# Kernel tuning notes

Measured on AMD Instinct MI355X. Metric: run time of the kernel, lower is better.

The kernel has to match this reference:

```python
import jax, jax.numpy as jnp
import numpy as np

B, N, C, H = 2, 2048, 1024, 16
D = C // H  # head_dim = 64
EPS = 1e-6


def rmsnorm(x, w, eps=EPS):
    # RMSNorm over last dim (head_dim), matching torch RMSNorm (computed in fp32)
    x32 = x.astype(jnp.float32)
    y = x32 * jax.lax.rsqrt(jnp.mean(x32 * x32, axis=-1, keepdims=True) + eps)
    return y.astype(x.dtype) * w


def setup_inputs() -> dict:
    key = jax.random.key(0)
    ks = jax.random.split(key, 4)
    return {
        "x": jax.random.normal(ks[0], (B, N, C), dtype=jnp.float32),
        "w_qkv": jax.random.normal(ks[1], (C, 3 * C), dtype=jnp.float32) * 0.02,
        "b_qkv": jnp.zeros((3 * C,), dtype=jnp.float32),
        "q_w": jnp.ones((D,), dtype=jnp.float32),
        "k_w": jnp.ones((D,), dtype=jnp.float32),
        "w_proj": jax.random.normal(ks[2], (C, C), dtype=jnp.float32) * 0.02,
        "b_proj": jnp.zeros((C,), dtype=jnp.float32),
    }


def reference(x, w_qkv, b_qkv, q_w, k_w, w_proj, b_proj):
    b, n, c = x.shape
    h, d = H, c // H
    # QKV projection -> [3, B, H, N, D]
    qkv = (x @ w_qkv + b_qkv).reshape(b, n, 3, h, d).transpose(2, 0, 3, 1, 4)
    q, k, v = qkv[0], qkv[1], qkv[2]
    # per-head RMSNorm on q/k (qk_norm=True, use_rmsnorm=True)
    q = rmsnorm(q, q_w)
    k = rmsnorm(k, k_w)
    # scaled dot-product attention (scale = head_dim**-0.5, no dropout at eval)
    scale = d ** -0.5
    attn = jax.nn.softmax(jnp.einsum('bhqd,bhkd->bhqk', q, k) * scale, axis=-1)
    out = jnp.einsum('bhqk,bhkd->bhqd', attn, v)  # [B,H,N,D]
    out = out.transpose(0, 2, 1, 3).reshape(b, n, c)
    return out @ w_proj + b_proj
```

## Files before the change

kernel.cpp:

```cpp
#include <hip/hip_runtime.h>

typedef unsigned short u16;
typedef unsigned int u32;
typedef float f4 __attribute__((ext_vector_type(4)));
typedef __bf16 b8 __attribute__((ext_vector_type(8)));
typedef _Float16 h4 __attribute__((ext_vector_type(4)));
typedef __fp16 hp2 __attribute__((ext_vector_type(2)));

#if __has_builtin(__builtin_amdgcn_exp2f)
#define EXP2(x) __builtin_amdgcn_exp2f(x)
#else
#define EXP2(x) exp2f(x)
#endif

__device__ __forceinline__ u16 f2bf(float f) {
  unsigned u = __float_as_uint(f);
  u += 0x7fffu + ((u >> 16) & 1u);
  return (u16)(u >> 16);
}
__device__ __forceinline__ float bf2f(u16 h) {
  return __uint_as_float(((unsigned)h) << 16);
}

__global__ void k_convert_all(const float* __restrict__ x,
                              const float* __restrict__ w_qkv,
                              const float* __restrict__ w_proj,
                              u16* __restrict__ xb, u16* __restrict__ wqkT,
                              u16* __restrict__ wpjT) {
  __shared__ u16 t[64][65];
  int bid = blockIdx.x;
  if (bid < 2048) {
    int i = (bid * 256 + threadIdx.x) * 8;
    float4 a = *(const float4*)(x + i);
    float4 b = *(const float4*)(x + i + 4);
    union { u16 h[8]; uint4 v; } r;
    r.h[0] = f2bf(a.x); r.h[1] = f2bf(a.y); r.h[2] = f2bf(a.z); r.h[3] = f2bf(a.w);
    r.h[4] = f2bf(b.x); r.h[5] = f2bf(b.y); r.h[6] = f2bf(b.z); r.h[7] = f2bf(b.w);
    *(uint4*)(xb + i) = r.v;
    return;
  }
  const float* w; u16* wT; int Ncols, Krows, bx, by;
  if (bid < 2816) { int l = bid - 2048; w = w_qkv; wT = wqkT; Ncols = 3072; Krows = 1024; bx = l % 48; by = l / 48; }
  else            { int l = bid - 2816; w = w_proj; wT = wpjT; Ncols = 1024; Krows = 1024; bx = l & 15; by = l >> 4; }
  int n0 = bx * 64, k0 = by * 64;
#pragma unroll
  for (int it = 0; it < 16; ++it) {
    int e = it * 256 + threadIdx.x;
    int r = e >> 6, c = e & 63;
    t[r][c] = f2bf(w[(size_t)(k0 + r) * Ncols + n0 + c]);
  }
  __syncthreads();
#pragma unroll
  for (int it = 0; it < 16; ++it) {
    int e = it * 256 + threadIdx.x;
    int r = e >> 6, c = e & 63;
    wT[(size_t)(n0 + r) * Krows + k0 + c] = t[c][r];
  }
}

__global__ __launch_bounds__(256, 3) void k_gemm_qkv(
    const u16* __restrict__ A, const u16* __restrict__ Bt,
    const float* __restrict__ bias,
    u16* __restrict__ oq, u16* __restrict__ ok, u16* __restrict__ ov,
    const float* __restrict__ qw, const float* __restrict__ kw,
    int K) {
  __shared__ u16 lA[128 * 32];
  __shared__ u16 lB[128 * 32];
  const int tid = threadIdx.x;
  const int lane = tid & 63, lrow = lane & 15, lq = lane >> 4;
  const int wave = tid >> 6;
  const int bm = blockIdx.y * 128, bn = blockIdx.x * 128;
  const int wm = (wave >> 1) * 64, wn = (wave & 1) * 64;

  const int ch0 = tid, ch1 = 256 + tid;
  const u16* ap0 = A + (size_t)(bm + (ch0 >> 2)) * K + (ch0 & 3) * 8;
  const u16* ap1 = A + (size_t)(bm + (ch1 >> 2)) * K + (ch1 & 3) * 8;
  const u16* bp0 = Bt + (size_t)(bn + (ch0 >> 2)) * K + (ch0 & 3) * 8;
  const u16* bp1 = Bt + (size_t)(bn + (ch1 >> 2)) * K + (ch1 & 3) * 8;
  u16* lAw0 = lA + ch0 * 8; u16* lAw1 = lA + ch1 * 8;
  u16* lBw0 = lB + ch0 * 8; u16* lBw1 = lB + ch1 * 8;

  uint4 pA0 = *(const uint4*)ap0, pA1 = *(const uint4*)ap1;
  uint4 pB0 = *(const uint4*)bp0, pB1 = *(const uint4*)bp1;

  f4 acc[4][4] = {};
  const int iters = K >> 5;
  for (int it = 0; it < iters; ++it) {
    *(uint4*)lAw0 = pA0; *(uint4*)lAw1 = pA1;
    *(uint4*)lBw0 = pB0; *(uint4*)lBw1 = pB1;
    __syncthreads();
    if (it + 1 < iters) {
      ap0 += 32; ap1 += 32; bp0 += 32; bp1 += 32;
      pA0 = *(const uint4*)ap0; pA1 = *(const uint4*)ap1;
      pB0 = *(const uint4*)bp0; pB1 = *(const uint4*)bp1;
    }
    b8 af[4], bf[4];
#pragma unroll
    for (int i = 0; i < 4; ++i)
      af[i] = *(const b8*)(lA + (wm + i * 16 + lrow) * 32 + lq * 8);
#pragma unroll
    for (int j = 0; j < 4; ++j)
      bf[j] = *(const b8*)(lB + (wn + j * 16 + lrow) * 32 + lq * 8);
#pragma unroll
    for (int i = 0; i < 4; ++i)
#pragma unroll
      for (int j = 0; j < 4; ++j)
        acc[i][j] = __builtin_amdgcn_mfma_f32_16x16x32_bf16(af[i], bf[j], acc[i][j], 0, 0, 0);
    __syncthreads();
  }

  float bv[4];
#pragma unroll
  for (int j = 0; j < 4; ++j) bv[j] = bias[bn + wn + j * 16 + lrow];

  const float CS = 0.125f * 1.44269504088896340736f;
  const int n0w = bn + wn;
  const int sec = n0w >> 10;
  const int h = (n0w >> 6) & 15;
#pragma unroll
  for (int i = 0; i < 4; ++i) {
    float v[4][4];
#pragma unroll
    for (int j = 0; j < 4; ++j)
#pragma unroll
      for (int r = 0; r < 4; ++r) v[j][r] = acc[i][j][r] + bv[j];
    if (sec < 2) {
      u16* dst = sec == 0 ? oq : ok;
      const float* w = sec == 0 ? qw : kw;
      float ex = sec == 0 ? CS : 1.0f;
#pragma unroll
      for (int r = 0; r < 4; ++r) {
        float ss = v[0][r] * v[0][r] + v[1][r] * v[1][r] +
                   v[2][r] * v[2][r] + v[3][r] * v[3][r];
        ss += __shfl_xor(ss, 1, 64); ss += __shfl_xor(ss, 2, 64);
        ss += __shfl_xor(ss, 4, 64); ss += __shfl_xor(ss, 8, 64);
        float sc = rsqrtf(ss * (1.0f / 64.0f) + 1e-6f) * ex;
        int m = bm + wm + i * 16 + lq * 4 + r;
        int bb = m >> 11, ns = m & 2047;
        u16* rowp = dst + ((size_t)(bb * 16 + h) * 2048 + ns) * 64;
#pragma unroll
        for (int j = 0; j < 4; ++j) {
          int d = j * 16 + lrow;
          rowp[d] = f2bf(v[j][r] * sc * w[d]);
        }
      }
    } else {
      int m0 = bm + wm + i * 16 + lq * 4;
      int bb = m0 >> 11, ns = m0 & 2047;
#pragma unroll
      for (int j = 0; j < 4; ++j) {
        int d = j * 16 + lrow;
        union { _Float16 hh[4]; uint2 u; } pk;
#pragma unroll
        for (int r = 0; r < 4; ++r) pk.hh[r] = (_Float16)v[j][r];
        *(uint2*)(ov + ((size_t)(bb * 16 + h) * 64 + d) * 2048 + ns) = pk.u;
      }
    }
  }
}

__global__ __launch_bounds__(256, 4) void k_gemm2(
    const u16* __restrict__ A, const u16* __restrict__ Bt,
    const float* __restrict__ bias, float* __restrict__ outF,
    int K, int Ncols) {
  __shared__ u16 lA[64 * 32];
  __shared__ u16 lB[128 * 32];
  const int tid = threadIdx.x;
  const int lane = tid & 63, lrow = lane & 15, lq = lane >> 4;
  const int wave = tid >> 6;
  const int bm = blockIdx.y * 64, bn = blockIdx.x * 128;
  const int wm = (wave >> 1) * 32, wn = (wave & 1) * 64;

  const int cha = tid;
  const int ch0 = tid, ch1 = 256 + tid;
  const u16* ap = A + (size_t)(bm + (cha >> 2)) * K + (cha & 3) * 8;
  const u16* bp0 = Bt + (size_t)(bn + (ch0 >> 2)) * K + (ch0 & 3) * 8;
  const u16* bp1 = Bt + (size_t)(bn + (ch1 >> 2)) * K + (ch1 & 3) * 8;
  u16* lAw = lA + cha * 8;
  u16* lBw0 = lB + ch0 * 8; u16* lBw1 = lB + ch1 * 8;

  uint4 pA = *(const uint4*)ap;
  uint4 pB0 = *(const uint4*)bp0, pB1 = *(const uint4*)bp1;

  f4 acc[2][4] = {};
  const int iters = K >> 5;
  for (int it = 0; it < iters; ++it) {
    *(uint4*)lAw = pA;
    *(uint4*)lBw0 = pB0; *(uint4*)lBw1 = pB1;
    __syncthreads();
    if (it + 1 < iters) {
      ap += 32; bp0 += 32; bp1 += 32;
      pA = *(const uint4*)ap;
      pB0 = *(const uint4*)bp0; pB1 = *(const uint4*)bp1;
    }
    b8 af[2], bf[4];
#pragma unroll
    for (int i = 0; i < 2; ++i)
      af[i] = *(const b8*)(lA + (wm + i * 16 + lrow) * 32 + lq * 8);
#pragma unroll
    for (int j = 0; j < 4; ++j)
      bf[j] = *(const b8*)(lB + (wn + j * 16 + lrow) * 32 + lq * 8);
#pragma unroll
    for (int i = 0; i < 2; ++i)
#pragma unroll
      for (int j = 0; j < 4; ++j)
        acc[i][j] = __builtin_amdgcn_mfma_f32_16x16x32_bf16(af[i], bf[j], acc[i][j], 0, 0, 0);
    __syncthreads();
  }
#pragma unroll
  for (int i = 0; i < 2; ++i)
#pragma unroll
    for (int j = 0; j < 4; ++j) {
      int n = bn + wn + j * 16 + lrow;
      float bv = bias[n];
#pragma unroll
      for (int r = 0; r < 4; ++r) {
        int m = bm + wm + i * 16 + lq * 4 + r;
        outF[(size_t)m * Ncols + n] = acc[i][j][r] + bv;
      }
    }
}

__global__ __launch_bounds__(512, 4) void k_attn(
    const u16* __restrict__ qb, const u16* __restrict__ kb,
    const u16* __restrict__ vt, u16* __restrict__ ao) {
  __shared__ u16 lK[128 * 72];
  __shared__ u16 lV[64 * 140];
  const int bh = blockIdx.y;
  const int q0 = blockIdx.x * 128;
  const int tid = threadIdx.x, wave = tid >> 6, lane = tid & 63;
  const int lrow = lane & 15, lq = lane >> 4;
  const int wq = wave * 16;

  b8 qf[2];
#pragma unroll
  for (int ks = 0; ks < 2; ++ks)
    qf[ks] = *(const b8*)(qb + ((size_t)bh * 2048 + q0 + wq + lrow) * 64 + ks * 32 + lq * 8);

  f4 o[4] = {};
  f4 lacc = {};
  h4 ones;
  ones[0] = (_Float16)1.0f; ones[1] = (_Float16)1.0f;
  ones[2] = (_Float16)1.0f; ones[3] = (_Float16)1.0f;

  const int ch0 = tid, ch1 = 512 + tid;
  const u16* kp0 = kb + (size_t)bh * 2048 * 64 + (size_t)(ch0 >> 3) * 64 + (ch0 & 7) * 8;
  const u16* kp1 = kb + (size_t)bh * 2048 * 64 + (size_t)(ch1 >> 3) * 64 + (ch1 & 7) * 8;
  const u16* vp0 = vt + (size_t)bh * 64 * 2048 + (size_t)(ch0 >> 4) * 2048 + (ch0 & 15) * 8;
  const u16* vp1 = vt + (size_t)bh * 64 * 2048 + (size_t)(ch1 >> 4) * 2048 + (ch1 & 15) * 8;
  u16* lKw0 = lK + (ch0 >> 3) * 72 + (ch0 & 7) * 8;
  u16* lKw1 = lK + (ch1 >> 3) * 72 + (ch1 & 7) * 8;
  u16* lVw0 = lV + (ch0 >> 4) * 140 + (ch0 & 15) * 8;
  u16* lVw1 = lV + (ch1 >> 4) * 140 + (ch1 & 15) * 8;

  uint4 pK0, pK1, pV0, pV1;
  pK0 = *(const uint4*)kp0; pK1 = *(const uint4*)kp1;
  pV0 = *(const uint4*)vp0; pV1 = *(const uint4*)vp1;

  for (int it = 0; it < 16; ++it) {
    *(uint4*)lKw0 = pK0;
    *(uint4*)lKw1 = pK1;
    *(uint2*)lVw0 = make_uint2(pV0.x, pV0.y);
    *(uint2*)(lVw0 + 4) = make_uint2(pV0.z, pV0.w);
    *(uint2*)lVw1 = make_uint2(pV1.x, pV1.y);
    *(uint2*)(lVw1 + 4) = make_uint2(pV1.z, pV1.w);
    __syncthreads();

    if (it < 15) {
      kp0 += 128 * 64; kp1 += 128 * 64; vp0 += 128; vp1 += 128;
      pK0 = *(const uint4*)kp0; pK1 = *(const uint4*)kp1;
      pV0 = *(const uint4*)vp0; pV1 = *(const uint4*)vp1;
    }

    f4 st[8] = {};
#pragma unroll
    for (int ks = 0; ks < 2; ++ks)
#pragma unroll
      for (int kt = 0; kt < 8; ++kt) {
        b8 kf = *(const b8*)(lK + (kt * 16 + lrow) * 72 + ks * 32 + lq * 8);
        st[kt] = __builtin_amdgcn_mfma_f32_16x16x32_bf16(kf, qf[ks], st[kt], 0, 0, 0);
      }

    h4 pf[8];
#pragma unroll
    for (int kt = 0; kt < 8; ++kt) {
      union { hp2 p2[2]; h4 v; } cv;
      cv.p2[0] = __builtin_amdgcn_cvt_pkrtz(EXP2(st[kt][0]), EXP2(st[kt][1]));
      cv.p2[1] = __builtin_amdgcn_cvt_pkrtz(EXP2(st[kt][2]), EXP2(st[kt][3]));
      pf[kt] = cv.v;
    }

#pragma unroll
    for (int kt = 0; kt < 8; ++kt) {
      lacc = __builtin_amdgcn_mfma_f32_16x16x16f16(ones, pf[kt], lacc, 0, 0, 0);
#pragma unroll
      for (int dt = 0; dt < 4; ++dt) {
        h4 va = *(const h4*)(lV + (dt * 16 + lrow) * 140 + kt * 16 + lq * 4);
        o[dt] = __builtin_amdgcn_mfma_f32_16x16x16f16(va, pf[kt], o[dt], 0, 0, 0);
      }
    }
    __syncthreads();
  }

  float inv = 1.0f / lacc[0];

  const int bb = bh >> 4, h = bh & 15;
  int q = q0 + wq + lrow;
#pragma unroll
  for (int dt = 0; dt < 4; ++dt) {
    union { u16 h2[4]; uint2 v; } r;
#pragma unroll
    for (int rr = 0; rr < 4; ++rr) r.h2[rr] = f2bf(o[dt][rr] * inv);
    *(uint2*)(ao + ((size_t)bb * 2048 + q) * 1024 + h * 64 + dt * 16 + lq * 4) = r.v;
  }
}

extern "C" void kernel_launch(void* const* d_in, const int* in_sizes, int n_in,
                              void* d_out, int out_size, void* d_ws, size_t ws_size,
                              hipStream_t stream) {
  const float* x      = (const float*)d_in[0];
  const float* w_qkv  = (const float*)d_in[1];
  const float* b_qkv  = (const float*)d_in[2];
  const float* q_w    = (const float*)d_in[3];
  const float* k_w    = (const float*)d_in[4];
  const float* w_proj = (const float*)d_in[5];
  const float* b_proj = (const float*)d_in[6];
  float* out = (float*)d_out;

  u16* xb   = (u16*)d_ws;
  u16* wqkT = xb + 4194304;
  u16* wpjT = wqkT + 3145728;
  u16* qb   = wpjT + 1048576;
  u16* kb   = qb + 4194304;
  u16* vtb  = kb + 4194304;
  u16* ao   = xb;

  k_convert_all<<<3072, 256, 0, stream>>>(x, w_qkv, w_proj, xb, wqkT, wpjT);
  k_gemm_qkv<<<dim3(24, 32), 256, 0, stream>>>(xb, wqkT, b_qkv, qb, kb, vtb, q_w, k_w, 1024);
  k_attn<<<dim3(16, 32), 512, 0, stream>>>(qb, kb, vtb, ao);
  k_gemm2<<<dim3(8, 64), 256, 0, stream>>>(ao, wpjT, b_proj, out, 1024, 1024);
}
```

Baseline: 193.3 us.

## Double attention KV tile to 256 keys and vectorize weight transpose stores

The attention kernel now stages 256 keys of K and V per iteration instead of 128 and processes them in two halves. This halves the number of barrier pairs and loop iterations, and lengthens each register-prefetch batch. In exchange it uses more LDS per block, about 70KB, which can cut how many blocks fit on a CU, and it needs more prefetch registers. The weight-transpose kernel also packs four bf16 values into 8-byte stores instead of writing scalar 2-byte ones.

```diff
diff --git a/kernel.cpp b/kernel.cpp
--- a/kernel.cpp
+++ b/kernel.cpp
@@ -51,10 +51,13 @@
   }
   __syncthreads();
 #pragma unroll
-  for (int it = 0; it < 16; ++it) {
+  for (int it = 0; it < 4; ++it) {
     int e = it * 256 + threadIdx.x;
-    int r = e >> 6, c = e & 63;
-    wT[(size_t)(n0 + r) * Krows + k0 + c] = t[c][r];
+    int r = e >> 4, c0 = (e & 15) * 4;
+    union { u16 h[4]; uint2 v; } pk;
+    pk.h[0] = t[c0][r]; pk.h[1] = t[c0 + 1][r];
+    pk.h[2] = t[c0 + 2][r]; pk.h[3] = t[c0 + 3][r];
+    *(uint2*)(wT + (size_t)(n0 + r) * Krows + k0 + c0) = pk.v;
   }
 }
 
@@ -224,8 +227,8 @@
 __global__ __launch_bounds__(512, 4) void k_attn(
     const u16* __restrict__ qb, const u16* __restrict__ kb,
     const u16* __restrict__ vt, u16* __restrict__ ao) {
-  __shared__ u16 lK[128 * 72];
-  __shared__ u16 lV[64 * 140];
+  __shared__ u16 lK[256 * 72];
+  __shared__ u16 lV[64 * 268];
   const int bh = blockIdx.y;
   const int q0 = blockIdx.x * 128;
   const int tid = threadIdx.x, wave = tid >> 6, lane = tid & 63;
@@ -243,60 +246,65 @@
   ones[0] = (_Float16)1.0f; ones[1] = (_Float16)1.0f;
   ones[2] = (_Float16)1.0f; ones[3] = (_Float16)1.0f;
 
-  const int ch0 = tid, ch1 = 512 + tid;
-  const u16* kp0 = kb + (size_t)bh * 2048 * 64 + (size_t)(ch0 >> 3) * 64 + (ch0 & 7) * 8;
-  const u16* kp1 = kb + (size_t)bh * 2048 * 64 + (size_t)(ch1 >> 3) * 64 + (ch1 & 7) * 8;
-  const u16* vp0 = vt + (size_t)bh * 64 * 2048 + (size_t)(ch0 >> 4) * 2048 + (ch0 & 15) * 8;
-  const u16* vp1 = vt + (size_t)bh * 64 * 2048 + (size_t)(ch1 >> 4) * 2048 + (ch1 & 15) * 8;
-  u16* lKw0 = lK + (ch0 >> 3) * 72 + (ch0 & 7) * 8;
-  u16* lKw1 = lK + (ch1 >> 3) * 72 + (ch1 & 7) * 8;
-  u16* lVw0 = lV + (ch0 >> 4) * 140 + (ch0 & 15) * 8;
-  u16* lVw1 = lV + (ch1 >> 4) * 140 + (ch1 & 15) * 8;
-
-  uint4 pK0, pK1, pV0, pV1;
-  pK0 = *(const uint4*)kp0; pK1 = *(const uint4*)kp1;
-  pV0 = *(const uint4*)vp0; pV1 = *(const uint4*)vp1;
-
-  for (int it = 0; it < 16; ++it) {
-    *(uint4*)lKw0 = pK0;
-    *(uint4*)lKw1 = pK1;
-    *(uint2*)lVw0 = make_uint2(pV0.x, pV0.y);
-    *(uint2*)(lVw0 + 4) = make_uint2(pV0.z, pV0.w);
-    *(uint2*)lVw1 = make_uint2(pV1.x, pV1.y);
-    *(uint2*)(lVw1 + 4) = make_uint2(pV1.z, pV1.w);
-    __syncthreads();
-
-    if (it < 15) {
-      kp0 += 128 * 64; kp1 += 128 * 64; vp0 += 128; vp1 += 128;
-      pK0 = *(const uint4*)kp0; pK1 = *(const uint4*)kp1;
-      pV0 = *(const uint4*)vp0; pV1 = *(const uint4*)vp1;
-    }
-
-    f4 st[8] = {};
-#pragma unroll
-    for (int ks = 0; ks < 2; ++ks)
+  const u16* kp[4]; const u16* vp[4];
+  u16* lKw[4]; u16* lVw[4];
+#pragma unroll
+  for (int s = 0; s < 4; ++s) {
+    int ch = s * 512 + tid;
+    int kr = ch >> 3, kc = ch & 7;
+    kp[s] = kb + (size_t)bh * 2048 * 64 + (size_t)kr * 64 + kc * 8;
+    lKw[s] = lK + kr * 72 + kc * 8;
+    int vr = ch >> 5, vc = ch & 31;
+    vp[s] = vt + (size_t)bh * 64 * 2048 + (size_t)vr * 2048 + vc * 8;
+    lVw[s] = lV + vr * 268 + vc * 8;
+  }
+  uint4 pK[4], pV[4];
+#pragma unroll
+  for (int s = 0; s < 4; ++s) { pK[s] = *(const uint4*)kp[s]; pV[s] = *(const uint4*)vp[s]; }
+
+  for (int it = 0; it < 8; ++it) {
+#pragma unroll
+    for (int s = 0; s < 4; ++s) {
+      *(uint4*)lKw[s] = pK[s];
+      *(uint2*)lVw[s] = make_uint2(pV[s].x, pV[s].y);
+      *(uint2*)(lVw[s] + 4) = make_uint2(pV[s].z, pV[s].w);
+    }
+    __syncthreads();
+
+    if (it < 7) {
+#pragma unroll
+      for (int s = 0; s < 4; ++s) {
+        kp[s] += 256 * 64; vp[s] += 256;
+        pK[s] = *(const uint4*)kp[s]; pV[s] = *(const uint4*)vp[s];
+      }
+    }
+
+#pragma unroll
+    for (int half = 0; half < 2; ++half) {
+      f4 st[8] = {};
+#pragma unroll
+      for (int ks = 0; ks < 2; ++ks)
+#pragma unroll
+        for (int kt = 0; kt < 8; ++kt) {
+          b8 kf = *(const b8*)(lK + ((half * 8 + kt) * 16 + lrow) * 72 + ks * 32 + lq * 8);
+          st[kt] = __builtin_amdgcn_mfma_f32_16x16x32_bf16(kf, qf[ks], st[kt], 0, 0, 0);
+        }
+      h4 pf[8];
 #pragma unroll
       for (int kt = 0; kt < 8; ++kt) {
-        b8 kf = *(const b8*)(lK + (kt * 16 + lrow) * 72 + ks * 32 + lq * 8);
-        st[kt] = __builtin_amdgcn_mfma_f32_16x16x32_bf16(kf, qf[ks], st[kt], 0, 0, 0);
-      }
-
-    h4 pf[8];
-#pragma unroll
-    for (int kt = 0; kt < 8; ++kt) {
-      union { hp2 p2[2]; h4 v; } cv;
-      cv.p2[0] = __builtin_amdgcn_cvt_pkrtz(EXP2(st[kt][0]), EXP2(st[kt][1]));
-      cv.p2[1] = __builtin_amdgcn_cvt_pkrtz(EXP2(st[kt][2]), EXP2(st[kt][3]));
-      pf[kt] = cv.v;
-    }
-
-#pragma unroll
-    for (int kt = 0; kt < 8; ++kt) {
-      lacc = __builtin_amdgcn_mfma_f32_16x16x16f16(ones, pf[kt], lacc, 0, 0, 0);
-#pragma unroll
-      for (int dt = 0; dt < 4; ++dt) {
-        h4 va = *(const h4*)(lV + (dt * 16 + lrow) * 140 + kt * 16 + lq * 4);
-        o[dt] = __builtin_amdgcn_mfma_f32_16x16x16f16(va, pf[kt], o[dt], 0, 0, 0);
+        union { hp2 p2[2]; h4 v; } cv;
+        cv.p2[0] = __builtin_amdgcn_cvt_pkrtz(EXP2(st[kt][0]), EXP2(st[kt][1]));
+        cv.p2[1] = __builtin_amdgcn_cvt_pkrtz(EXP2(st[kt][2]), EXP2(st[kt][3]));
+        pf[kt] = cv.v;
+      }
+#pragma unroll
+      for (int kt = 0; kt < 8; ++kt) {
+        lacc = __builtin_amdgcn_mfma_f32_16x16x16f16(ones, pf[kt], lacc, 0, 0, 0);
+#pragma unroll
+        for (int dt = 0; dt < 4; ++dt) {
+          h4 va = *(const h4*)(lV + (dt * 16 + lrow) * 268 + (half * 8 + kt) * 16 + lq * 4);
+          o[dt] = __builtin_amdgcn_mfma_f32_16x16x16f16(va, pf[kt], o[dt], 0, 0, 0);
+        }
       }
     }
     __syncthreads();
```

Result: slower. 219.3 us (+13.5%).

## Double-buffer LDS tiles in GEMM and attention loops, vectorize weight transpose stores

Applied to the files above, without the earlier changes.

Gives the two GEMM kernels and the attention kernel two shared-memory buffers that alternate each iteration. This removes the second barrier per loop iteration and lets the next global prefetch be issued before the barrier. The weight-transpose store in the conversion kernel now writes four bf16 values per 8-byte store instead of one scalar u16 per thread. The cost is doubled LDS use per block, which may lower occupancy, notably for the 512-thread attention kernel.

```diff
diff --git a/kernel.cpp b/kernel.cpp
--- a/kernel.cpp
+++ b/kernel.cpp
@@ -51,10 +51,13 @@
   }
   __syncthreads();
 #pragma unroll
-  for (int it = 0; it < 16; ++it) {
+  for (int it = 0; it < 4; ++it) {
     int e = it * 256 + threadIdx.x;
-    int r = e >> 6, c = e & 63;
-    wT[(size_t)(n0 + r) * Krows + k0 + c] = t[c][r];
+    int r = e >> 4, c0 = (e & 15) * 4;
+    union { u16 h[4]; uint2 v; } pk;
+    pk.h[0] = t[c0][r]; pk.h[1] = t[c0 + 1][r];
+    pk.h[2] = t[c0 + 2][r]; pk.h[3] = t[c0 + 3][r];
+    *(uint2*)(wT + (size_t)(n0 + r) * Krows + k0 + c0) = pk.v;
   }
 }
 
@@ -64,8 +67,8 @@
     u16* __restrict__ oq, u16* __restrict__ ok, u16* __restrict__ ov,
     const float* __restrict__ qw, const float* __restrict__ kw,
     int K) {
-  __shared__ u16 lA[128 * 32];
-  __shared__ u16 lB[128 * 32];
+  __shared__ u16 lA[2][128 * 32];
+  __shared__ u16 lB[2][128 * 32];
   const int tid = threadIdx.x;
   const int lane = tid & 63, lrow = lane & 15, lq = lane >> 4;
   const int wave = tid >> 6;
@@ -77,8 +80,6 @@
   const u16* ap1 = A + (size_t)(bm + (ch1 >> 2)) * K + (ch1 & 3) * 8;
   const u16* bp0 = Bt + (size_t)(bn + (ch0 >> 2)) * K + (ch0 & 3) * 8;
   const u16* bp1 = Bt + (size_t)(bn + (ch1 >> 2)) * K + (ch1 & 3) * 8;
-  u16* lAw0 = lA + ch0 * 8; u16* lAw1 = lA + ch1 * 8;
-  u16* lBw0 = lB + ch0 * 8; u16* lBw1 = lB + ch1 * 8;
 
   uint4 pA0 = *(const uint4*)ap0, pA1 = *(const uint4*)ap1;
   uint4 pB0 = *(const uint4*)bp0, pB1 = *(const uint4*)bp1;
@@ -86,27 +87,27 @@
   f4 acc[4][4] = {};
   const int iters = K >> 5;
   for (int it = 0; it < iters; ++it) {
-    *(uint4*)lAw0 = pA0; *(uint4*)lAw1 = pA1;
-    *(uint4*)lBw0 = pB0; *(uint4*)lBw1 = pB1;
-    __syncthreads();
+    const int s = it & 1;
+    *(uint4*)(lA[s] + ch0 * 8) = pA0; *(uint4*)(lA[s] + ch1 * 8) = pA1;
+    *(uint4*)(lB[s] + ch0 * 8) = pB0; *(uint4*)(lB[s] + ch1 * 8) = pB1;
     if (it + 1 < iters) {
       ap0 += 32; ap1 += 32; bp0 += 32; bp1 += 32;
       pA0 = *(const uint4*)ap0; pA1 = *(const uint4*)ap1;
       pB0 = *(const uint4*)bp0; pB1 = *(const uint4*)bp1;
     }
+    __syncthreads();
     b8 af[4], bf[4];
 #pragma unroll
     for (int i = 0; i < 4; ++i)
-      af[i] = *(const b8*)(lA + (wm + i * 16 + lrow) * 32 + lq * 8);
+      af[i] = *(const b8*)(lA[s] + (wm + i * 16 + lrow) * 32 + lq * 8);
 #pragma unroll
     for (int j = 0; j < 4; ++j)
-      bf[j] = *(const b8*)(lB + (wn + j * 16 + lrow) * 32 + lq * 8);
+      bf[j] = *(const b8*)(lB[s] + (wn + j * 16 + lrow) * 32 + lq * 8);
 #pragma unroll
     for (int i = 0; i < 4; ++i)
 #pragma unroll
       for (int j = 0; j < 4; ++j)
         acc[i][j] = __builtin_amdgcn_mfma_f32_16x16x32_bf16(af[i], bf[j], acc[i][j], 0, 0, 0);
-    __syncthreads();
   }
 
   float bv[4];
@@ -163,8 +164,8 @@
     const u16* __restrict__ A, const u16* __restrict__ Bt,
     const float* __restrict__ bias, float* __restrict__ outF,
     int K, int Ncols) {
-  __shared__ u16 lA[64 * 32];
-  __shared__ u16 lB[128 * 32];
+  __shared__ u16 lA[2][64 * 32];
+  __shared__ u16 lB[2][128 * 32];
   const int tid = threadIdx.x;
   const int lane = tid & 63, lrow = lane & 15, lq = lane >> 4;
   const int wave = tid >> 6;
@@ -176,8 +177,6 @@
   const u16* ap = A + (size_t)(bm + (cha >> 2)) * K + (cha & 3) * 8;
   const u16* bp0 = Bt + (size_t)(bn + (ch0 >> 2)) * K + (ch0 & 3) * 8;
   const u16* bp1 = Bt + (size_t)(bn + (ch1 >> 2)) * K + (ch1 & 3) * 8;
-  u16* lAw = lA + cha * 8;
-  u16* lBw0 = lB + ch0 * 8; u16* lBw1 = lB + ch1 * 8;
 
   uint4 pA = *(const uint4*)ap;
   uint4 pB0 = *(const uint4*)bp0, pB1 = *(const uint4*)bp1;
@@ -185,27 +184,27 @@
   f4 acc[2][4] = {};
   const int iters = K >> 5;
   for (int it = 0; it < iters; ++it) {
-    *(uint4*)lAw = pA;
-    *(uint4*)lBw0 = pB0; *(uint4*)lBw1 = pB1;
-    __syncthreads();
+    const int s = it & 1;
+    *(uint4*)(lA[s] + cha * 8) = pA;
+    *(uint4*)(lB[s] + ch0 * 8) = pB0; *(uint4*)(lB[s] + ch1 * 8) = pB1;
     if (it + 1 < iters) {
       ap += 32; bp0 += 32; bp1 += 32;
       pA = *(const uint4*)ap;
       pB0 = *(const uint4*)bp0; pB1 = *(const uint4*)bp1;
     }
+    __syncthreads();
     b8 af[2], bf[4];
 #pragma unroll
     for (int i = 0; i < 2; ++i)
-      af[i] = *(const b8*)(lA + (wm + i * 16 + lrow) * 32 + lq * 8);
+      af[i] = *(const b8*)(lA[s] + (wm + i * 16 + lrow) * 32 + lq * 8);
 #pragma unroll
     for (int j = 0; j < 4; ++j)
-      bf[j] = *(const b8*)(lB + (wn + j * 16 + lrow) * 32 + lq * 8);
+      bf[j] = *(const b8*)(lB[s] + (wn + j * 16 + lrow) * 32 + lq * 8);
 #pragma unroll
     for (int i = 0; i < 2; ++i)
 #pragma unroll
       for (int j = 0; j < 4; ++j)
         acc[i][j] = __builtin_amdgcn_mfma_f32_16x16x32_bf16(af[i], bf[j], acc[i][j], 0, 0, 0);
-    __syncthreads();
   }
 #pragma unroll
   for (int i = 0; i < 2; ++i)
@@ -224,8 +223,8 @@
 __global__ __launch_bounds__(512, 4) void k_attn(
     const u16* __restrict__ qb, const u16* __restrict__ kb,
     const u16* __restrict__ vt, u16* __restrict__ ao) {
-  __shared__ u16 lK[128 * 72];
-  __shared__ u16 lV[64 * 140];
+  __shared__ u16 lK[2][128 * 72];
+  __shared__ u16 lV[2][64 * 140];
   const int bh = blockIdx.y;
   const int q0 = blockIdx.x * 128;
   const int tid = threadIdx.x, wave = tid >> 6, lane = tid & 63;
@@ -248,36 +247,37 @@
   const u16* kp1 = kb + (size_t)bh * 2048 * 64 + (size_t)(ch1 >> 3) * 64 + (ch1 & 7) * 8;
   const u16* vp0 = vt + (size_t)bh * 64 * 2048 + (size_t)(ch0 >> 4) * 2048 + (ch0 & 15) * 8;
   const u16* vp1 = vt + (size_t)bh * 64 * 2048 + (size_t)(ch1 >> 4) * 2048 + (ch1 & 15) * 8;
-  u16* lKw0 = lK + (ch0 >> 3) * 72 + (ch0 & 7) * 8;
-  u16* lKw1 = lK + (ch1 >> 3) * 72 + (ch1 & 7) * 8;
-  u16* lVw0 = lV + (ch0 >> 4) * 140 + (ch0 & 15) * 8;
-  u16* lVw1 = lV + (ch1 >> 4) * 140 + (ch1 & 15) * 8;
+  const int kO0 = (ch0 >> 3) * 72 + (ch0 & 7) * 8;
+  const int kO1 = (ch1 >> 3) * 72 + (ch1 & 7) * 8;
+  const int vO0 = (ch0 >> 4) * 140 + (ch0 & 15) * 8;
+  const int vO1 = (ch1 >> 4) * 140 + (ch1 & 15) * 8;
 
   uint4 pK0, pK1, pV0, pV1;
   pK0 = *(const uint4*)kp0; pK1 = *(const uint4*)kp1;
   pV0 = *(const uint4*)vp0; pV1 = *(const uint4*)vp1;
 
   for (int it = 0; it < 16; ++it) {
-    *(uint4*)lKw0 = pK0;
-    *(uint4*)lKw1 = pK1;
-    *(uint2*)lVw0 = make_uint2(pV0.x, pV0.y);
-    *(uint2*)(lVw0 + 4) = make_uint2(pV0.z, pV0.w);
-    *(uint2*)lVw1 = make_uint2(pV1.x, pV1.y);
-    *(uint2*)(lVw1 + 4) = make_uint2(pV1.z, pV1.w);
-    __syncthreads();
+    const int s = it & 1;
+    *(uint4*)(lK[s] + kO0) = pK0;
+    *(uint4*)(lK[s] + kO1) = pK1;
+    *(uint2*)(lV[s] + vO0) = make_uint2(pV0.x, pV0.y);
+    *(uint2*)(lV[s] + vO0 + 4) = make_uint2(pV0.z, pV0.w);
+    *(uint2*)(lV[s] + vO1) = make_uint2(pV1.x, pV1.y);
+    *(uint2*)(lV[s] + vO1 + 4) = make_uint2(pV1.z, pV1.w);
 
     if (it < 15) {
       kp0 += 128 * 64; kp1 += 128 * 64; vp0 += 128; vp1 += 128;
       pK0 = *(const uint4*)kp0; pK1 = *(const uint4*)kp1;
       pV0 = *(const uint4*)vp0; pV1 = *(const uint4*)vp1;
     }
+    __syncthreads();
 
     f4 st[8] = {};
 #pragma unroll
     for (int ks = 0; ks < 2; ++ks)
 #pragma unroll
       for (int kt = 0; kt < 8; ++kt) {
-        b8 kf = *(const b8*)(lK + (kt * 16 + lrow) * 72 + ks * 32 + lq * 8);
+        b8 kf = *(const b8*)(lK[s] + (kt * 16 + lrow) * 72 + ks * 32 + lq * 8);
         st[kt] = __builtin_amdgcn_mfma_f32_16x16x32_bf16(kf, qf[ks], st[kt], 0, 0, 0);
       }
 
@@ -295,11 +295,10 @@
       lacc = __builtin_amdgcn_mfma_f32_16x16x16f16(ones, pf[kt], lacc, 0, 0, 0);
 #pragma unroll
       for (int dt = 0; dt < 4; ++dt) {
-        h4 va = *(const h4*)(lV + (dt * 16 + lrow) * 140 + kt * 16 + lq * 4);
+        h4 va = *(const h4*)(lV[s] + (dt * 16 + lrow) * 140 + kt * 16 + lq * 4);
         o[dt] = __builtin_amdgcn_mfma_f32_16x16x16f16(va, pf[kt], o[dt], 0, 0, 0);
       }
     }
-    __syncthreads();
   }
 
   float inv = 1.0f / lacc[0];
```

Result: no change. 192.5 us (-0.4%).
